# Kernel tuning notes

Measured on AMD Instinct MI355X. Metric: run time of the kernel, lower is better.

The kernel has to match this reference:

```python
import jax, jax.numpy as jnp
import numpy as np

N = 100000      # nodes
E = 1600000     # edges (before self-loops)
F_IN = 128      # dataset.num_node_features
H, C = 8, 8     # heads, hid
D = H * C       # 64, concat output dim
G = 64          # graphs in batch
N_CLS = 10
SLOPE = 0.2     # PyG GATConv negative_slope default


def setup_inputs() -> dict:
    key = jax.random.key(0)
    ks = jax.random.split(key, 16)
    s = 0.1
    return {
        "x": jax.random.normal(ks[0], (N, F_IN), jnp.float32),
        "edge_index": jax.random.randint(ks[1], (2, E), 0, N, jnp.int32),
        "batch": jnp.sort(jax.random.randint(ks[2], (N,), 0, G, jnp.int32)),
        "W1": jax.random.normal(ks[3], (F_IN, D), jnp.float32) * s,
        "a1_src": jax.random.normal(ks[4], (H, C), jnp.float32) * s,
        "a1_dst": jax.random.normal(ks[5], (H, C), jnp.float32) * s,
        "b1": jnp.zeros((D,), jnp.float32),
        "W2": jax.random.normal(ks[6], (D, D), jnp.float32) * s,
        "a2_src": jax.random.normal(ks[7], (H, C), jnp.float32) * s,
        "a2_dst": jax.random.normal(ks[8], (H, C), jnp.float32) * s,
        "b2": jnp.zeros((D,), jnp.float32),
        "W3": jax.random.normal(ks[9], (D, D), jnp.float32) * s,
        "a3_src": jax.random.normal(ks[10], (H, C), jnp.float32) * s,
        "a3_dst": jax.random.normal(ks[11], (H, C), jnp.float32) * s,
        "b3": jnp.zeros((D,), jnp.float32),
        "lin_W": jax.random.normal(ks[12], (D, N_CLS), jnp.float32) * s,
        "lin_b": jnp.zeros((N_CLS,), jnp.float32),
    }


def _gat_conv(h_in, src, dst, W, a_src, a_dst, b):
    # h: [N, H, C] per-head projected features
    h = (h_in @ W).reshape(N, H, C)
    al_src = jnp.einsum('nhc,hc->nh', h, a_src)  # [N, H]
    al_dst = jnp.einsum('nhc,hc->nh', h, a_dst)
    e = al_src[src] + al_dst[dst]                # [E', H]
    e = jnp.where(e > 0, e, SLOPE * e)           # LeakyReLU
    # segment softmax over incoming edges of each dst node
    m = jax.ops.segment_max(e, dst, num_segments=N)          # every node has a self-loop
    e = jnp.exp(e - m[dst])
    denom = jax.ops.segment_sum(e, dst, num_segments=N)
    alpha = e / denom[dst]                        # [E', H]
    out = jax.ops.segment_sum(h[src] * alpha[:, :, None], dst, num_segments=N)
    return out.reshape(N, D) + b


def reference(x, edge_index, batch, W1, a1_src, a1_dst, b1,
              W2, a2_src, a2_dst, b2, W3, a3_src, a3_dst, b3, lin_W, lin_b):
    # PyG GATConv add_self_loops=True
    loop = jnp.arange(N, dtype=edge_index.dtype)
    src = jnp.concatenate([edge_index[0], loop])
    dst = jnp.concatenate([edge_index[1], loop])

    h = jax.nn.elu(_gat_conv(x, src, dst, W1, a1_src, a1_dst, b1))
    h = jax.nn.elu(_gat_conv(h, src, dst, W2, a2_src, a2_dst, b2))
    h = jax.nn.elu(_gat_conv(h, src, dst, W3, a3_src, a3_dst, b3))

    # global mean pool over graph assignment
    sums = jax.ops.segment_sum(h, batch, num_segments=G)          # [G, D]
    cnts = jax.ops.segment_sum(jnp.ones((N,), h.dtype), batch, num_segments=G)
    pooled = sums / jnp.maximum(cnts, 1.0)[:, None]

    return pooled @ lin_W + lin_b  # [G, N_CLS]
```

## Files before the change

kernel.cpp:

```cpp
#include <hip/hip_runtime.h>
#include <math.h>

#define NN 100000
#define EE 1600000
#define GG 64
#define NCLS 10

#define BSH 8
#define NB 391
#define BCAP 4608
#define EPS 4096
#define CAPS 5120

typedef unsigned int uint32;

__device__ __forceinline__ unsigned short f2bf(float f) {
    unsigned u = __float_as_uint(f);
    unsigned r = (u + 0x7fffu + ((u >> 16) & 1u)) >> 16;
    return (unsigned short)r;
}

__device__ __forceinline__ float bf2f(unsigned short h) {
    return __uint_as_float((unsigned)h << 16);
}


__global__ __launch_bounds__(512) void bscatter_kernel(
    const int* __restrict__ src, const int* __restrict__ dst,
    int* __restrict__ bfill, uint32* __restrict__ bpack, int n) {
    __shared__ int hist[512], gbase[512], lbase[512], cnt2[512];
    __shared__ int wtot[8];
    __shared__ uint32 lsd[EPS];
    __shared__ unsigned short bkt[EPS];
    int tid = threadIdx.x;
    int lane = tid & 63, wv = tid >> 6;
    int e0 = blockIdx.x * EPS;
    int e1 = min(e0 + EPS, n);

    hist[tid] = 0;
    cnt2[tid] = 0;
    __syncthreads();
    for (int e = e0 + tid; e < e1; e += 512) atomicAdd(&hist[dst[e] >> BSH], 1);
    __syncthreads();
    int h = hist[tid];
    int inc = h;
#pragma unroll
    for (int off = 1; off < 64; off <<= 1) {
        int t = __shfl_up(inc, off);
        if (lane >= off) inc += t;
    }
    if (lane == 63) wtot[wv] = inc;
    __syncthreads();
    if (tid < 8) {
        int t = wtot[tid];
#pragma unroll
        for (int off = 1; off < 8; off <<= 1) {
            int u = __shfl_up(t, off, 8);
            if (tid >= off) t += u;
        }
        wtot[tid] = t;
    }
    __syncthreads();
    if (wv > 0) inc += wtot[wv - 1];
    int lb = inc - h;
    lbase[tid] = lb;
    int go = h > 0 ? atomicAdd(&bfill[tid], h) : 0;
    gbase[tid] = tid * BCAP + go - lb;
    __syncthreads();
    for (int e = e0 + tid; e < e1; e += 512) {
        int s = src[e], dd = dst[e];
        int b = dd >> BSH;
        int r = atomicAdd(&cnt2[b], 1);
        int slot = lbase[b] + r;
        lsd[slot] = ((uint32)s << 8) | (uint32)(dd & 255);
        bkt[slot] = (unsigned short)b;
    }
    __syncthreads();
    int m = e1 - e0;
    for (int i = tid; i < m; i += 512)
        bpack[gbase[bkt[i]] + i] = lsd[i];
}

__global__ __launch_bounds__(256) void bsort_kernel(
    const uint32* __restrict__ bpack, const int* __restrict__ bfill,
    int2* __restrict__ rpe, int* __restrict__ col) {
    __shared__ int cnt[256], cnt2[256];
    __shared__ int wtot[4];
    __shared__ int stage[CAPS];
    int b = blockIdx.x;
    int tid = threadIdx.x;
    int ebeg = b * BCAP;
    int sz = bfill[b];
    int n0 = b << BSH;
    int nn = min(256, NN - n0);

    cnt[tid] = 0;
    cnt2[tid] = 0;
    __syncthreads();
    const uint4* bq = (const uint4*)(bpack + ebeg);
    int nq = sz >> 2;
    for (int i = tid; i < nq; i += 256) {
        uint4 p = bq[i];
        atomicAdd(&cnt[p.x & 255u], 1);
        atomicAdd(&cnt[p.y & 255u], 1);
        atomicAdd(&cnt[p.z & 255u], 1);
        atomicAdd(&cnt[p.w & 255u], 1);
    }
    for (int e = (nq << 2) + tid; e < sz; e += 256)
        atomicAdd(&cnt[bpack[ebeg + e] & 255u], 1);
    __syncthreads();
    int lane = tid & 63, wv = tid >> 6;
    int c = cnt[tid];
    int inc = c;
#pragma unroll
    for (int off = 1; off < 64; off <<= 1) {
        int t = __shfl_up(inc, off);
        if (lane >= off) inc += t;
    }
    if (lane == 63) wtot[wv] = inc;
    __syncthreads();
    if (tid < 4) {
        int t = wtot[tid];
#pragma unroll
        for (int off = 1; off < 4; off <<= 1) {
            int u = __shfl_up(t, off, 4);
            if (tid >= off) t += u;
        }
        wtot[tid] = t;
    }
    __syncthreads();
    if (wv > 0) inc += wtot[wv - 1];
    int excl = inc - c;
    cnt[tid] = excl;
    if (tid < nn) {
        rpe[n0 + tid] = make_int2(ebeg + excl, ebeg + inc);
    }
    __syncthreads();
    bool fits = sz <= CAPS;
    for (int i = tid; i < nq; i += 256) {
        uint4 p = bq[i];
        int d0 = (int)(p.x & 255u), d1 = (int)(p.y & 255u);
        int d2 = (int)(p.z & 255u), d3 = (int)(p.w & 255u);
        int p0 = cnt[d0] + atomicAdd(&cnt2[d0], 1);
        int p1 = cnt[d1] + atomicAdd(&cnt2[d1], 1);
        int p2 = cnt[d2] + atomicAdd(&cnt2[d2], 1);
        int p3 = cnt[d3] + atomicAdd(&cnt2[d3], 1);
        if (fits) {
            stage[p0] = (int)(p.x >> 8); stage[p1] = (int)(p.y >> 8);
            stage[p2] = (int)(p.z >> 8); stage[p3] = (int)(p.w >> 8);
        } else {
            col[ebeg + p0] = (int)(p.x >> 8); col[ebeg + p1] = (int)(p.y >> 8);
            col[ebeg + p2] = (int)(p.z >> 8); col[ebeg + p3] = (int)(p.w >> 8);
        }
    }
    for (int e = (nq << 2) + tid; e < sz; e += 256) {
        uint32 p = bpack[ebeg + e];
        int dl = (int)(p & 255u);
        int pos = cnt[dl] + atomicAdd(&cnt2[dl], 1);
        if (fits) stage[pos] = (int)(p >> 8);
        else col[ebeg + pos] = (int)(p >> 8);
    }
    __syncthreads();
    if (fits) {
        uint4* colq = (uint4*)(col + ebeg);
        const uint4* stq = (const uint4*)stage;
        for (int i = tid; i < nq; i += 256) colq[i] = stq[i];
        for (int i = (nq << 2) + tid; i < sz; i += 256) col[ebeg + i] = stage[i];
    }
}


template <int K, bool BF16IN>
__global__ __launch_bounds__(256) void gemm_al_kernel(
    const void* __restrict__ Xv, const float* __restrict__ W,
    const float* __restrict__ a_src, const float* __restrict__ a_dst,
    unsigned short* __restrict__ H, float* __restrict__ ALs, float* __restrict__ ALd,
    int nrows) {
    const int KC = 64;
    const int KP = KC + 4;
    __shared__ float Xs[64 * (KC + 4)];
    __shared__ float Ws[K * 64];
    int tid = threadIdx.x;
    int r0 = blockIdx.x * 64;
    int validRows = min(64, nrows - r0);

    {
        const float4* Wg = (const float4*)W;
        float4* Ws4 = (float4*)Ws;
        for (int i = tid; i < K * 16; i += 256) Ws4[i] = Wg[i];
    }

    int cg = tid & 15, rg = tid >> 4;
    int rbase = rg * 4;
    float4 acc0 = make_float4(0.f, 0.f, 0.f, 0.f);
    float4 acc1 = acc0, acc2 = acc0, acc3 = acc0;

    for (int kc = 0; kc < K; kc += KC) {
        __syncthreads();
        for (int i = tid; i < 64 * 16; i += 256) {
            int row = i >> 4, q = i & 15;
            float4 v;
            if (row < validRows) {
                if constexpr (BF16IN) {
                    const uint2* Xg2 = (const uint2*)Xv;
                    uint2 p = Xg2[(size_t)(r0 + row) * (K / 4) + (kc >> 2) + q];
                    v.x = __uint_as_float(p.x << 16);
                    v.y = __uint_as_float(p.x & 0xffff0000u);
                    v.z = __uint_as_float(p.y << 16);
                    v.w = __uint_as_float(p.y & 0xffff0000u);
                } else {
                    const float4* Xg = (const float4*)Xv;
                    v = Xg[(size_t)(r0 + row) * (K / 4) + (kc >> 2) + q];
                }
            } else {
                v = make_float4(0.f, 0.f, 0.f, 0.f);
            }
            *(float4*)&Xs[row * KP + q * 4] = v;
        }
        __syncthreads();

#pragma unroll 2
        for (int k = 0; k < KC; k += 4) {
            float4 x0 = *(const float4*)&Xs[(rbase + 0) * KP + k];
            float4 x1 = *(const float4*)&Xs[(rbase + 1) * KP + k];
            float4 x2 = *(const float4*)&Xs[(rbase + 2) * KP + k];
            float4 x3 = *(const float4*)&Xs[(rbase + 3) * KP + k];
            float4 w0 = *(const float4*)&Ws[(kc + k + 0) * 64 + 4 * cg];
            float4 w1 = *(const float4*)&Ws[(kc + k + 1) * 64 + 4 * cg];
            float4 w2 = *(const float4*)&Ws[(kc + k + 2) * 64 + 4 * cg];
            float4 w3 = *(const float4*)&Ws[(kc + k + 3) * 64 + 4 * cg];
#define FMA4(A, S, WV) \
            A.x = fmaf(S, WV.x, A.x); A.y = fmaf(S, WV.y, A.y); \
            A.z = fmaf(S, WV.z, A.z); A.w = fmaf(S, WV.w, A.w)
            FMA4(acc0, x0.x, w0); FMA4(acc1, x1.x, w0); FMA4(acc2, x2.x, w0); FMA4(acc3, x3.x, w0);
            FMA4(acc0, x0.y, w1); FMA4(acc1, x1.y, w1); FMA4(acc2, x2.y, w1); FMA4(acc3, x3.y, w1);
            FMA4(acc0, x0.z, w2); FMA4(acc1, x1.z, w2); FMA4(acc2, x2.z, w2); FMA4(acc3, x3.z, w2);
            FMA4(acc0, x0.w, w3); FMA4(acc1, x1.w, w3); FMA4(acc2, x2.w, w3); FMA4(acc3, x3.w, w3);
#undef FMA4
        }
    }

    int hh = cg >> 1;
    float4 as4 = ((const float4*)a_src)[cg];
    float4 ad4 = ((const float4*)a_dst)[cg];
    float4 accs[4] = {acc0, acc1, acc2, acc3};
#pragma unroll
    for (int i = 0; i < 4; ++i) {
        int r = r0 + rbase + i;
        if (r < nrows) {
            ushort4 p;
            p.x = f2bf(accs[i].x); p.y = f2bf(accs[i].y);
            p.z = f2bf(accs[i].z); p.w = f2bf(accs[i].w);
            ((ushort4*)H)[(size_t)r * 16 + cg] = p;
            float ps = accs[i].x * as4.x + accs[i].y * as4.y +
                       accs[i].z * as4.z + accs[i].w * as4.w;
            float pd = accs[i].x * ad4.x + accs[i].y * ad4.y +
                       accs[i].z * ad4.z + accs[i].w * ad4.w;
            ps += __shfl_xor(ps, 1);
            pd += __shfl_xor(pd, 1);
            if ((cg & 1) == 0) {
                ALs[r * 8 + hh] = ps;
                ALd[r * 8 + hh] = pd;
            }
        }
    }
}


__global__ __launch_bounds__(256, 6) void agg_kernel(
    const unsigned short* __restrict__ H, const float* __restrict__ ALs,
    const float* __restrict__ ALd, const int2* __restrict__ rpe,
    const int* __restrict__ col,
    const float* __restrict__ bias, unsigned short* __restrict__ Out, int n) {
    int tid = threadIdx.x;
    int lane = tid & 63;
    int slot = lane >> 4;
    int epar = (lane >> 3) & 1;
    int head = lane & 7;
    int wid = blockIdx.x * 4 + (tid >> 6);
    int d = wid * 4 + slot;
    bool active = d < n;
    if (!active) d = n - 1;
    const uint4* __restrict__ Hq = (const uint4*)H;

    float ad = ALd[d * 8 + head];
    float acc0 = 0.f, acc1 = 0.f, acc2 = 0.f, acc3 = 0.f;
    float acc4 = 0.f, acc5 = 0.f, acc6 = 0.f, acc7 = 0.f;
    float wsum = 0.f;

#define FMA8(U, W) { \
    acc0 = fmaf(W, __uint_as_float((U).x << 16), acc0); \
    acc1 = fmaf(W, __uint_as_float((U).x & 0xffff0000u), acc1); \
    acc2 = fmaf(W, __uint_as_float((U).y << 16), acc2); \
    acc3 = fmaf(W, __uint_as_float((U).y & 0xffff0000u), acc3); \
    acc4 = fmaf(W, __uint_as_float((U).z << 16), acc4); \
    acc5 = fmaf(W, __uint_as_float((U).z & 0xffff0000u), acc5); \
    acc6 = fmaf(W, __uint_as_float((U).w << 16), acc6); \
    acc7 = fmaf(W, __uint_as_float((U).w & 0xffff0000u), acc7); }

    if (epar == 0) {
        uint4 u = Hq[(size_t)d * 8 + head];
        float e = ALs[d * 8 + head] + ad;
        e = fmaxf(e, 0.2f * e);
        float w = __expf(e);
        FMA8(u, w);
        wsum = w;
    }

    int2 kk = rpe[d];
    int k = kk.x + epar, kend = kk.y;
    for (; k + 6 < kend; k += 8) {
        int s0 = __builtin_nontemporal_load(&col[k]);
        int s1 = __builtin_nontemporal_load(&col[k + 2]);
        int s2 = __builtin_nontemporal_load(&col[k + 4]);
        int s3 = __builtin_nontemporal_load(&col[k + 6]);
        uint4 u0 = Hq[(size_t)s0 * 8 + head];
        uint4 u1 = Hq[(size_t)s1 * 8 + head];
        uint4 u2 = Hq[(size_t)s2 * 8 + head];
        uint4 u3 = Hq[(size_t)s3 * 8 + head];
        float a0 = ALs[s0 * 8 + head];
        float a1 = ALs[s1 * 8 + head];
        float a2 = ALs[s2 * 8 + head];
        float a3 = ALs[s3 * 8 + head];
        float e0 = a0 + ad; e0 = fmaxf(e0, 0.2f * e0); float w0 = __expf(e0);
        float e1 = a1 + ad; e1 = fmaxf(e1, 0.2f * e1); float w1 = __expf(e1);
        float e2 = a2 + ad; e2 = fmaxf(e2, 0.2f * e2); float w2 = __expf(e2);
        float e3 = a3 + ad; e3 = fmaxf(e3, 0.2f * e3); float w3 = __expf(e3);
        FMA8(u0, w0);
        FMA8(u1, w1);
        FMA8(u2, w2);
        FMA8(u3, w3);
        wsum += (w0 + w1) + (w2 + w3);
    }
    if (k + 2 < kend) {
        int s0 = __builtin_nontemporal_load(&col[k]);
        int s1 = __builtin_nontemporal_load(&col[k + 2]);
        uint4 u0 = Hq[(size_t)s0 * 8 + head];
        uint4 u1 = Hq[(size_t)s1 * 8 + head];
        float a0 = ALs[s0 * 8 + head];
        float a1 = ALs[s1 * 8 + head];
        float e0 = a0 + ad; e0 = fmaxf(e0, 0.2f * e0); float w0 = __expf(e0);
        float e1 = a1 + ad; e1 = fmaxf(e1, 0.2f * e1); float w1 = __expf(e1);
        FMA8(u0, w0);
        FMA8(u1, w1);
        wsum += w0 + w1;
        k += 4;
    }
    if (k < kend) {
        int s = __builtin_nontemporal_load(&col[k]);
        uint4 u = Hq[(size_t)s * 8 + head];
        float a = ALs[s * 8 + head];
        float e = a + ad; e = fmaxf(e, 0.2f * e);
        float w = __expf(e);
        FMA8(u, w);
        wsum += w;
    }
#undef FMA8

    wsum += __shfl_xor(wsum, 8);
    acc0 += __shfl_xor(acc0, 8);
    acc1 += __shfl_xor(acc1, 8);
    acc2 += __shfl_xor(acc2, 8);
    acc3 += __shfl_xor(acc3, 8);
    acc4 += __shfl_xor(acc4, 8);
    acc5 += __shfl_xor(acc5, 8);
    acc6 += __shfl_xor(acc6, 8);
    acc7 += __shfl_xor(acc7, 8);

    if (active && epar == 0) {
        float inv = 1.f / wsum;
        float4 b0 = ((const float4*)bias)[head * 2];
        float4 b1 = ((const float4*)bias)[head * 2 + 1];
        float o0, o1, o2, o3, o4, o5, o6, o7;
        o0 = fmaf(acc0, inv, b0.x); o0 = o0 > 0.f ? o0 : expm1f(o0);
        o1 = fmaf(acc1, inv, b0.y); o1 = o1 > 0.f ? o1 : expm1f(o1);
        o2 = fmaf(acc2, inv, b0.z); o2 = o2 > 0.f ? o2 : expm1f(o2);
        o3 = fmaf(acc3, inv, b0.w); o3 = o3 > 0.f ? o3 : expm1f(o3);
        o4 = fmaf(acc4, inv, b1.x); o4 = o4 > 0.f ? o4 : expm1f(o4);
        o5 = fmaf(acc5, inv, b1.y); o5 = o5 > 0.f ? o5 : expm1f(o5);
        o6 = fmaf(acc6, inv, b1.z); o6 = o6 > 0.f ? o6 : expm1f(o6);
        o7 = fmaf(acc7, inv, b1.w); o7 = o7 > 0.f ? o7 : expm1f(o7);
        uint4 pk;
        pk.x = (uint32)f2bf(o0) | ((uint32)f2bf(o1) << 16);
        pk.y = (uint32)f2bf(o2) | ((uint32)f2bf(o3) << 16);
        pk.z = (uint32)f2bf(o4) | ((uint32)f2bf(o5) << 16);
        pk.w = (uint32)f2bf(o6) | ((uint32)f2bf(o7) << 16);
        ((uint4*)Out)[(size_t)d * 8 + head] = pk;
    }
}


__global__ void pool_kernel(const unsigned short* __restrict__ H, const int* __restrict__ batch,
                            float* __restrict__ sums, float* __restrict__ cnt, int n) {
    int gw = (int)((blockIdx.x * blockDim.x + threadIdx.x) >> 6);
    int lane = threadIdx.x & 63;
    int n0 = gw * 64;
    if (n0 >= n) return;
    int n1 = min(n0 + 64, n);
    int curb = batch[n0];
    float local = 0.f, c_local = 0.f;
    for (int i = n0; i < n1; ++i) {
        int b = batch[i];
        if (b != curb) {
            atomicAdd(&sums[curb * 64 + lane], local);
            if (lane == 0) atomicAdd(&cnt[curb], c_local);
            local = 0.f;
            c_local = 0.f;
            curb = b;
        }
        local += bf2f(H[(size_t)i * 64 + lane]);
        c_local += 1.f;
    }
    atomicAdd(&sums[curb * 64 + lane], local);
    if (lane == 0) atomicAdd(&cnt[curb], c_local);
}

__global__ void final_kernel(const float* __restrict__ sums, const float* __restrict__ cnt,
                             const float* __restrict__ W, const float* __restrict__ b,
                             float* __restrict__ out) {
    int t = blockIdx.x * blockDim.x + threadIdx.x;
    if (t >= GG * NCLS) return;
    int g = t / NCLS, k = t % NCLS;
    float c = cnt[g];
    if (c < 1.f) c = 1.f;
    float inv = 1.f / c;
    float acc = b[k];
#pragma unroll
    for (int cc = 0; cc < 64; ++cc)
        acc = fmaf(sums[g * 64 + cc] * inv, W[cc * NCLS + k], acc);
    out[t] = acc;
}


extern "C" void kernel_launch(void* const* d_in, const int* in_sizes, int n_in,
                              void* d_out, int out_size, void* d_ws, size_t ws_size,
                              hipStream_t stream) {
    const float* x    = (const float*)d_in[0];
    const int*   ei   = (const int*)d_in[1];
    const int*   batch = (const int*)d_in[2];
    const float* W1 = (const float*)d_in[3];
    const float* a1s = (const float*)d_in[4];
    const float* a1d = (const float*)d_in[5];
    const float* b1 = (const float*)d_in[6];
    const float* W2 = (const float*)d_in[7];
    const float* a2s = (const float*)d_in[8];
    const float* a2d = (const float*)d_in[9];
    const float* b2 = (const float*)d_in[10];
    const float* W3 = (const float*)d_in[11];
    const float* a3s = (const float*)d_in[12];
    const float* a3d = (const float*)d_in[13];
    const float* b3 = (const float*)d_in[14];
    const float* linW = (const float*)d_in[15];
    const float* linb = (const float*)d_in[16];
    float* out = (float*)d_out;

    char* ws = (char*)d_ws;
    size_t off = 0;
    auto alloc = [&](size_t bytes) -> void* {
        void* p = ws + off;
        off = (off + bytes + 255) & ~(size_t)255;
        return p;
    };
    unsigned short* hBf = (unsigned short*)alloc((size_t)NN * 64 * 2);
    unsigned short* hF16 = (unsigned short*)alloc((size_t)NN * 64 * 2);
    float* ALs    = (float*)alloc((size_t)NN * 8 * 4);
    float* ALd    = (float*)alloc((size_t)NN * 8 * 4);
    int2*  rpe    = (int2*)alloc((size_t)NN * 8);
    int*   bfill  = (int*)alloc((size_t)NB * 4);
    uint32* bpack = (uint32*)alloc((size_t)NB * BCAP * 4);
    int*   col    = (int*)alloc((size_t)NB * BCAP * 4);
    float* sums   = (float*)alloc((size_t)(GG * 64 + GG) * 4);
    float* gcnt   = sums + GG * 64;

    const int NBLK = (NN + 255) / 256;
    const int SB = (EE + EPS - 1) / EPS;

    hipMemsetAsync(bfill, 0, (size_t)NB * 4, stream);
    bscatter_kernel<<<SB, 512, 0, stream>>>(ei, ei + EE, bfill, bpack, EE);
    bsort_kernel<<<NB, 256, 0, stream>>>(bpack, bfill, rpe, col);

    const int GB = (NN + 63) / 64;
    const int AB = (NN + 15) / 16;

    gemm_al_kernel<128, false><<<GB, 256, 0, stream>>>(x, W1, a1s, a1d, hBf, ALs, ALd, NN);
    agg_kernel<<<AB, 256, 0, stream>>>(hBf, ALs, ALd, rpe, col, b1, hF16, NN);

    gemm_al_kernel<64, true><<<GB, 256, 0, stream>>>(hF16, W2, a2s, a2d, hBf, ALs, ALd, NN);
    agg_kernel<<<AB, 256, 0, stream>>>(hBf, ALs, ALd, rpe, col, b2, hF16, NN);

    gemm_al_kernel<64, true><<<GB, 256, 0, stream>>>(hF16, W3, a3s, a3d, hBf, ALs, ALd, NN);
    agg_kernel<<<AB, 256, 0, stream>>>(hBf, ALs, ALd, rpe, col, b3, hF16, NN);

    hipMemsetAsync(sums, 0, (size_t)(GG * 64 + GG) * 4, stream);
    pool_kernel<<<NBLK, 256, 0, stream>>>(hF16, batch, sums, gcnt, NN);
    final_kernel<<<3, 256, 0, stream>>>(sums, gcnt, linW, linb, out);
}
```

Measured before the change: 400.8 us.

## Fuse edge bucketing with layer-1 GEMM and pool with final linear

Merges the edge bucket-scatter and the first projection GEMM into one launch, splitting blocks by index so the two independent jobs run concurrently. The scatter chunk is halved so more blocks share the work. Pooling and the final linear layer become one kernel that uses a ticket counter so the last block computes the output. The two memsets are combined into one. This removes several launches and lets independent work overlap, at the cost of a larger shared-memory footprint per block and a different GEMM tile shape for layer 1.

```diff
diff --git a/kernel.cpp b/kernel.cpp
--- a/kernel.cpp
+++ b/kernel.cpp
@@ -9,8 +9,10 @@
 #define BSH 8
 #define NB 391
 #define BCAP 4608
-#define EPS 4096
+#define EPS 2048
+#define SBLK 782
 #define CAPS 5120
+#define GB 1563
 
 typedef unsigned int uint32;
 
@@ -25,61 +27,148 @@
 }
 
 
-__global__ __launch_bounds__(512) void bscatter_kernel(
+__global__ __launch_bounds__(512) void pre_kernel(
     const int* __restrict__ src, const int* __restrict__ dst,
-    int* __restrict__ bfill, uint32* __restrict__ bpack, int n) {
-    __shared__ int hist[512], gbase[512], lbase[512], cnt2[512];
-    __shared__ int wtot[8];
-    __shared__ uint32 lsd[EPS];
-    __shared__ unsigned short bkt[EPS];
+    int* __restrict__ bfill, uint32* __restrict__ bpack, int nE,
+    const float* __restrict__ X, const float* __restrict__ W,
+    const float* __restrict__ a_src, const float* __restrict__ a_dst,
+    unsigned short* __restrict__ H, float* __restrict__ ALs, float* __restrict__ ALd) {
+    __shared__ __align__(16) char smem[50176];
     int tid = threadIdx.x;
-    int lane = tid & 63, wv = tid >> 6;
-    int e0 = blockIdx.x * EPS;
-    int e1 = min(e0 + EPS, n);
-
-    hist[tid] = 0;
-    cnt2[tid] = 0;
-    __syncthreads();
-    for (int e = e0 + tid; e < e1; e += 512) atomicAdd(&hist[dst[e] >> BSH], 1);
-    __syncthreads();
-    int h = hist[tid];
-    int inc = h;
-#pragma unroll
-    for (int off = 1; off < 64; off <<= 1) {
-        int t = __shfl_up(inc, off);
-        if (lane >= off) inc += t;
-    }
-    if (lane == 63) wtot[wv] = inc;
-    __syncthreads();
-    if (tid < 8) {
-        int t = wtot[tid];
-#pragma unroll
-        for (int off = 1; off < 8; off <<= 1) {
-            int u = __shfl_up(t, off, 8);
-            if (tid >= off) t += u;
-        }
-        wtot[tid] = t;
-    }
-    __syncthreads();
-    if (wv > 0) inc += wtot[wv - 1];
-    int lb = inc - h;
-    lbase[tid] = lb;
-    int go = h > 0 ? atomicAdd(&bfill[tid], h) : 0;
-    gbase[tid] = tid * BCAP + go - lb;
-    __syncthreads();
-    for (int e = e0 + tid; e < e1; e += 512) {
-        int s = src[e], dd = dst[e];
-        int b = dd >> BSH;
-        int r = atomicAdd(&cnt2[b], 1);
-        int slot = lbase[b] + r;
-        lsd[slot] = ((uint32)s << 8) | (uint32)(dd & 255);
-        bkt[slot] = (unsigned short)b;
-    }
-    __syncthreads();
-    int m = e1 - e0;
-    for (int i = tid; i < m; i += 512)
-        bpack[gbase[bkt[i]] + i] = lsd[i];
-}
+
+    if (blockIdx.x < SBLK) {
+        int* hist  = (int*)smem;
+        int* gbase = hist + 512;
+        int* lbase = gbase + 512;
+        int* cnt2  = lbase + 512;
+        int* wtot  = cnt2 + 512;
+        uint32* lsd = (uint32*)(wtot + 8);
+        unsigned short* bkt = (unsigned short*)(lsd + EPS);
+
+        int lane = tid & 63, wv = tid >> 6;
+        int e0 = blockIdx.x * EPS;
+        int e1 = min(e0 + EPS, nE);
+
+        hist[tid] = 0;
+        cnt2[tid] = 0;
+        __syncthreads();
+        for (int e = e0 + tid; e < e1; e += 512) atomicAdd(&hist[dst[e] >> BSH], 1);
+        __syncthreads();
+        int h = hist[tid];
+        int inc = h;
+#pragma unroll
+        for (int off = 1; off < 64; off <<= 1) {
+            int t = __shfl_up(inc, off);
+            if (lane >= off) inc += t;
+        }
+        if (lane == 63) wtot[wv] = inc;
+        __syncthreads();
+        if (tid < 8) {
+            int t = wtot[tid];
+#pragma unroll
+            for (int off = 1; off < 8; off <<= 1) {
+                int u = __shfl_up(t, off, 8);
+                if (tid >= off) t += u;
+            }
+            wtot[tid] = t;
+        }
+        __syncthreads();
+        if (wv > 0) inc += wtot[wv - 1];
+        int lb = inc - h;
+        lbase[tid] = lb;
+        int go = h > 0 ? atomicAdd(&bfill[tid], h) : 0;
+        gbase[tid] = tid * BCAP + go - lb;
+        __syncthreads();
+        for (int e = e0 + tid; e < e1; e += 512) {
+            int s = src[e], dd = dst[e];
+            int b = dd >> BSH;
+            int r = atomicAdd(&cnt2[b], 1);
+            int slot = lbase[b] + r;
+            lsd[slot] = ((uint32)s << 8) | (uint32)(dd & 255);
+            bkt[slot] = (unsigned short)b;
+        }
+        __syncthreads();
+        int m = e1 - e0;
+        for (int i = tid; i < m; i += 512)
+            bpack[gbase[bkt[i]] + i] = lsd[i];
+    } else {
+        const int K = 128, KC = 64, KP = 68;
+        float* Xs = (float*)smem;
+        float* Ws = Xs + 64 * KP;
+        int r0 = (blockIdx.x - SBLK) * 64;
+        int validRows = min(64, NN - r0);
+
+        {
+            const float4* Wg = (const float4*)W;
+            float4* Ws4 = (float4*)Ws;
+            for (int i = tid; i < K * 16; i += 512) Ws4[i] = Wg[i];
+        }
+
+        int cg = tid & 15, rg = tid >> 4;
+        int rbase = rg * 2;
+        float4 acc0 = make_float4(0.f, 0.f, 0.f, 0.f);
+        float4 acc1 = acc0;
+
+        const float4* Xg = (const float4*)X;
+        const int QG = K / 4;
+
+        for (int kc = 0; kc < K; kc += KC) {
+            __syncthreads();
+            for (int i = tid; i < 64 * 16; i += 512) {
+                int row = i >> 4, q = i & 15;
+                float4 v = (row < validRows)
+                    ? Xg[(size_t)(r0 + row) * QG + (kc >> 2) + q]
+                    : make_float4(0.f, 0.f, 0.f, 0.f);
+                *(float4*)&Xs[row * KP + q * 4] = v;
+            }
+            __syncthreads();
+
+#pragma unroll 2
+            for (int k = 0; k < KC; k += 4) {
+                float4 x0 = *(const float4*)&Xs[(rbase + 0) * KP + k];
+                float4 x1 = *(const float4*)&Xs[(rbase + 1) * KP + k];
+                float4 w0 = *(const float4*)&Ws[(kc + k + 0) * 64 + 4 * cg];
+                float4 w1 = *(const float4*)&Ws[(kc + k + 1) * 64 + 4 * cg];
+                float4 w2 = *(const float4*)&Ws[(kc + k + 2) * 64 + 4 * cg];
+                float4 w3 = *(const float4*)&Ws[(kc + k + 3) * 64 + 4 * cg];
+#define FMA4(A, S, WV) \
+                A.x = fmaf(S, WV.x, A.x); A.y = fmaf(S, WV.y, A.y); \
+                A.z = fmaf(S, WV.z, A.z); A.w = fmaf(S, WV.w, A.w)
+                FMA4(acc0, x0.x, w0); FMA4(acc1, x1.x, w0);
+                FMA4(acc0, x0.y, w1); FMA4(acc1, x1.y, w1);
+                FMA4(acc0, x0.z, w2); FMA4(acc1, x1.z, w2);
+                FMA4(acc0, x0.w, w3); FMA4(acc1, x1.w, w3);
+#undef FMA4
+            }
+        }
+
+        int hh = cg >> 1;
+        float4 as4 = ((const float4*)a_src)[cg];
+        float4 ad4 = ((const float4*)a_dst)[cg];
+        float4 accs[2] = {acc0, acc1};
+#pragma unroll
+        for (int i = 0; i < 2; ++i) {
+            int r = r0 + rbase + i;
+            if (r < NN) {
+                ushort4 p;
+                p.x = f2bf(accs[i].x); p.y = f2bf(accs[i].y);
+                p.z = f2bf(accs[i].z); p.w = f2bf(accs[i].w);
+                ((ushort4*)H)[(size_t)r * 16 + cg] = p;
+                float ps = accs[i].x * as4.x + accs[i].y * as4.y +
+                           accs[i].z * as4.z + accs[i].w * as4.w;
+                float pd = accs[i].x * ad4.x + accs[i].y * ad4.y +
+                           accs[i].z * ad4.z + accs[i].w * ad4.w;
+                ps += __shfl_xor(ps, 1);
+                pd += __shfl_xor(pd, 1);
+                if ((cg & 1) == 0) {
+                    ALs[r * 8 + hh] = ps;
+                    ALd[r * 8 + hh] = pd;
+                }
+            }
+        }
+    }
+}
+
 
 __global__ __launch_bounds__(256) void bsort_kernel(
     const uint32* __restrict__ bpack, const int* __restrict__ bfill,
@@ -170,9 +259,9 @@
 }
 
 
-template <int K, bool BF16IN>
+template <int K>
 __global__ __launch_bounds__(256) void gemm_al_kernel(
-    const void* __restrict__ Xv, const float* __restrict__ W,
+    const unsigned short* __restrict__ Xv, const float* __restrict__ W,
     const float* __restrict__ a_src, const float* __restrict__ a_dst,
     unsigned short* __restrict__ H, float* __restrict__ ALs, float* __restrict__ ALd,
     int nrows) {
@@ -201,17 +290,12 @@
             int row = i >> 4, q = i & 15;
             float4 v;
             if (row < validRows) {
-                if constexpr (BF16IN) {
-                    const uint2* Xg2 = (const uint2*)Xv;
-                    uint2 p = Xg2[(size_t)(r0 + row) * (K / 4) + (kc >> 2) + q];
-                    v.x = __uint_as_float(p.x << 16);
-                    v.y = __uint_as_float(p.x & 0xffff0000u);
-                    v.z = __uint_as_float(p.y << 16);
-                    v.w = __uint_as_float(p.y & 0xffff0000u);
-                } else {
-                    const float4* Xg = (const float4*)Xv;
-                    v = Xg[(size_t)(r0 + row) * (K / 4) + (kc >> 2) + q];
-                }
+                const uint2* Xg2 = (const uint2*)Xv;
+                uint2 p = Xg2[(size_t)(r0 + row) * (K / 4) + (kc >> 2) + q];
+                v.x = __uint_as_float(p.x << 16);
+                v.y = __uint_as_float(p.x & 0xffff0000u);
+                v.z = __uint_as_float(p.y << 16);
+                v.w = __uint_as_float(p.y & 0xffff0000u);
             } else {
                 v = make_float4(0.f, 0.f, 0.f, 0.f);
             }
@@ -390,45 +474,56 @@
 }
 
 
-__global__ void pool_kernel(const unsigned short* __restrict__ H, const int* __restrict__ batch,
-                            float* __restrict__ sums, float* __restrict__ cnt, int n) {
-    int gw = (int)((blockIdx.x * blockDim.x + threadIdx.x) >> 6);
-    int lane = threadIdx.x & 63;
-    int n0 = gw * 64;
-    if (n0 >= n) return;
-    int n1 = min(n0 + 64, n);
-    int curb = batch[n0];
-    float local = 0.f, c_local = 0.f;
-    for (int i = n0; i < n1; ++i) {
-        int b = batch[i];
-        if (b != curb) {
-            atomicAdd(&sums[curb * 64 + lane], local);
-            if (lane == 0) atomicAdd(&cnt[curb], c_local);
-            local = 0.f;
-            c_local = 0.f;
-            curb = b;
-        }
-        local += bf2f(H[(size_t)i * 64 + lane]);
-        c_local += 1.f;
-    }
-    atomicAdd(&sums[curb * 64 + lane], local);
-    if (lane == 0) atomicAdd(&cnt[curb], c_local);
-}
-
-__global__ void final_kernel(const float* __restrict__ sums, const float* __restrict__ cnt,
-                             const float* __restrict__ W, const float* __restrict__ b,
-                             float* __restrict__ out) {
-    int t = blockIdx.x * blockDim.x + threadIdx.x;
-    if (t >= GG * NCLS) return;
-    int g = t / NCLS, k = t % NCLS;
-    float c = cnt[g];
-    if (c < 1.f) c = 1.f;
-    float inv = 1.f / c;
-    float acc = b[k];
-#pragma unroll
-    for (int cc = 0; cc < 64; ++cc)
-        acc = fmaf(sums[g * 64 + cc] * inv, W[cc * NCLS + k], acc);
-    out[t] = acc;
+__global__ __launch_bounds__(256) void poolfinal_kernel(
+    const unsigned short* __restrict__ H16, const int* __restrict__ batch,
+    float* __restrict__ sums, float* __restrict__ gcnt, int* __restrict__ ticket,
+    const float* __restrict__ linW, const float* __restrict__ linb,
+    float* __restrict__ out, int n) {
+    __shared__ int lflag;
+    int tid = threadIdx.x;
+    int lane = tid & 63;
+    int n0 = (blockIdx.x * 4 + (tid >> 6)) * 16;
+    if (n0 < n) {
+        int n1 = min(n0 + 16, n);
+        int curb = batch[n0];
+        float loc = 0.f, c = 0.f;
+        for (int i = n0; i < n1; ++i) {
+            int b = batch[i];
+            if (b != curb) {
+                atomicAdd(&sums[curb * 64 + lane], loc);
+                if (lane == 0) atomicAdd(&gcnt[curb], c);
+                loc = 0.f; c = 0.f; curb = b;
+            }
+            loc += bf2f(H16[(size_t)i * 64 + lane]);
+            c += 1.f;
+        }
+        atomicAdd(&sums[curb * 64 + lane], loc);
+        if (lane == 0) atomicAdd(&gcnt[curb], c);
+    }
+
+    __threadfence();
+    __syncthreads();
+    if (tid == 0) {
+        int t = __hip_atomic_fetch_add(ticket, 1, __ATOMIC_ACQ_REL, __HIP_MEMORY_SCOPE_AGENT);
+        lflag = (t == (int)gridDim.x - 1) ? 1 : 0;
+    }
+    __syncthreads();
+    if (lflag) {
+        for (int t2 = tid; t2 < GG * NCLS; t2 += 256) {
+            int g = t2 / NCLS, k = t2 % NCLS;
+            float c = __hip_atomic_load(&gcnt[g], __ATOMIC_RELAXED, __HIP_MEMORY_SCOPE_AGENT);
+            if (c < 1.f) c = 1.f;
+            float inv = 1.f / c;
+            float acc = linb[k];
+#pragma unroll
+            for (int cc = 0; cc < 64; ++cc) {
+                float s = __hip_atomic_load(&sums[g * 64 + cc], __ATOMIC_RELAXED,
+                                            __HIP_MEMORY_SCOPE_AGENT);
+                acc = fmaf(s * inv, linW[cc * NCLS + k], acc);
+            }
+            out[t2] = acc;
+        }
+    }
 }
 
 
@@ -461,37 +556,35 @@
         off = (off + bytes + 255) & ~(size_t)255;
         return p;
     };
-    unsigned short* hBf = (unsigned short*)alloc((size_t)NN * 64 * 2);
+    const size_t ZBYTES = (size_t)NB * 4 + (size_t)GG * 64 * 4 + (size_t)GG * 4 + 4;
+    char* zr = (char*)alloc(ZBYTES);
+    int*   bfill = (int*)zr;
+    float* sums  = (float*)(zr + (size_t)NB * 4);
+    float* gcnt  = sums + GG * 64;
+    int*   ticket = (int*)(gcnt + GG);
+
+    unsigned short* hBf  = (unsigned short*)alloc((size_t)NN * 64 * 2);
     unsigned short* hF16 = (unsigned short*)alloc((size_t)NN * 64 * 2);
-    float* ALs    = (float*)alloc((size_t)NN * 8 * 4);
-    float* ALd    = (float*)alloc((size_t)NN * 8 * 4);
-    int2*  rpe    = (int2*)alloc((size_t)NN * 8);
-    int*   bfill  = (int*)alloc((size_t)NB * 4);
+    float* ALs  = (float*)alloc((size_t)NN * 8 * 4);
+    float* ALd  = (float*)alloc((size_t)NN * 8 * 4);
+    int2*  rpe  = (int2*)alloc((size_t)NN * 8);
     uint32* bpack = (uint32*)alloc((size_t)NB * BCAP * 4);
-    int*   col    = (int*)alloc((size_t)NB * BCAP * 4);
-    float* sums   = (float*)alloc((size_t)(GG * 64 + GG) * 4);
-    float* gcnt   = sums + GG * 64;
-
-    const int NBLK = (NN + 255) / 256;
-    const int SB = (EE + EPS - 1) / EPS;
-
-    hipMemsetAsync(bfill, 0, (size_t)NB * 4, stream);
-    bscatter_kernel<<<SB, 512, 0, stream>>>(ei, ei + EE, bfill, bpack, EE);
+    int*   col  = (int*)alloc((size_t)NB * BCAP * 4);
+
+    hipMemsetAsync(zr, 0, ZBYTES, stream);
+
+    pre_kernel<<<SBLK + GB, 512, 0, stream>>>(ei, ei + EE, bfill, bpack, EE,
+                                              x, W1, a1s, a1d, hBf, ALs, ALd);
     bsort_kernel<<<NB, 256, 0, stream>>>(bpack, bfill, rpe, col);
 
-    const int GB = (NN + 63) / 64;
     const int AB = (NN + 15) / 16;
 
-    gemm_al_kernel<128, false><<<GB, 256, 0, stream>>>(x, W1, a1s, a1d, hBf, ALs, ALd, NN);
     agg_kernel<<<AB, 256, 0, stream>>>(hBf, ALs, ALd, rpe, col, b1, hF16, NN);
-
-    gemm_al_kernel<64, true><<<GB, 256, 0, stream>>>(hF16, W2, a2s, a2d, hBf, ALs, ALd, NN);
+    gemm_al_kernel<64><<<GB, 256, 0, stream>>>(hF16, W2, a2s, a2d, hBf, ALs, ALd, NN);
     agg_kernel<<<AB, 256, 0, stream>>>(hBf, ALs, ALd, rpe, col, b2, hF16, NN);
-
-    gemm_al_kernel<64, true><<<GB, 256, 0, stream>>>(hF16, W3, a3s, a3d, hBf, ALs, ALd, NN);
+    gemm_al_kernel<64><<<GB, 256, 0, stream>>>(hF16, W3, a3s, a3d, hBf, ALs, ALd, NN);
     agg_kernel<<<AB, 256, 0, stream>>>(hBf, ALs, ALd, rpe, col, b3, hF16, NN);
 
-    hipMemsetAsync(sums, 0, (size_t)(GG * 64 + GG) * 4, stream);
-    pool_kernel<<<NBLK, 256, 0, stream>>>(hF16, batch, sums, gcnt, NN);
-    final_kernel<<<3, 256, 0, stream>>>(sums, gcnt, linW, linb, out);
-}
+    poolfinal_kernel<<<GB, 256, 0, stream>>>(hF16, batch, sums, gcnt, ticket,
+                                             linW, linb, out, NN);
+}
```

Result: slower. 496.1 us (+23.8%).
